# Optimization experiments

Hardware: AMD Instinct MI355X
Metric: run time of the kernel (lower is better)

## Reference

```python
import jax, jax.numpy as jnp
import numpy as np

B, F, N_SP, VIS_DIM, DIM, HEADS = 2, 16, 784, 512, 512, 8


def setup_inputs() -> dict:
    key = jax.random.key(0)
    k0, k1, k2 = jax.random.split(key, 3)
    x = jax.random.normal(k0, (B, F * N_SP, VIS_DIM), dtype=jnp.float32)
    # QKV: nn.Linear(vis_dim, dim*3, bias=False) -> weight [3*dim, vis_dim]
    Wqkv = jax.random.normal(k1, (3 * DIM, VIS_DIM), dtype=jnp.float32) * 0.02
    # proj: nn.Linear(dim, vis_dim) -> weight [vis_dim, dim], bias [vis_dim]
    Wproj = jax.random.normal(k2, (VIS_DIM, DIM), dtype=jnp.float32) * 0.02
    bproj = jnp.zeros((VIS_DIM,), dtype=jnp.float32)
    return {"x": x, "Wqkv": Wqkv, "Wproj": Wproj, "bproj": bproj,
            "spatial": N_SP, "f": F, "n": N_SP}


def reference(x, Wqkv, Wproj, bproj, spatial, f, n):
    # Factorized (divided space-time) SPATIAL attention:
    # einops_from='b (f n) d', einops_to='(b f) n d' -- attention over n within each frame.
    h = HEADS
    b, seq, _ = x.shape  # seq = f * n
    dim = Wqkv.shape[0] // 3
    hd = dim // h
    scale = hd ** -0.5

    qkv = x @ Wqkv.T                             # [b, f*n, 3*dim]
    q, k, v = jnp.split(qkv, 3, axis=-1)
    rs = lambda t: t.reshape(b, f, n, h, hd)     # b (f n) (h d) -> b f n h d
    q = rs(q) * scale
    k = rs(k)
    v = rs(v)

    # scores over spatial tokens within each (batch, frame, head)
    attn = jax.nn.softmax(jnp.einsum('bfihd,bfjhd->bfhij', q, k), axis=-1)
    out = jnp.einsum('bfhij,bfjhd->bfihd', attn, v)   # [b, f, n, h, hd]
    out = out.reshape(b, seq, dim)               # merge heads + restore (f n)
    return out @ Wproj.T + bproj                 # [b, f*n, vis_dim]
```

## Files before the change

### kernel.cpp

```cpp
#include <hip/hip_runtime.h>
#include <hip/hip_bf16.h>
#include <stdint.h>

using bf16 = __hip_bfloat16;
typedef __bf16 bf16x8 __attribute__((ext_vector_type(8)));
typedef float f32x4  __attribute__((ext_vector_type(4)));
typedef float f32x16 __attribute__((ext_vector_type(16)));

#define NB 2
#define NF 16
#define NSP 784
#define SEQ 12544
#define MROWS 25088
#define QSCALE 0.18033688011112042f

__device__ inline void gload16(const void* g, void* l) {
    __builtin_amdgcn_global_load_lds(
        (const __attribute__((address_space(1))) unsigned int*)g,
        (__attribute__((address_space(3))) unsigned int*)l, 16, 0, 0);
}
__device__ inline ushort f2bu(float x) {
    union { bf16 b; ushort u; } c; c.b = __float2bfloat16(x); return c.u;
}

__global__ __launch_bounds__(256)
void cvt_x_kernel(const float* __restrict__ x, ushort* __restrict__ xb, int n4) {
    int i = blockIdx.x * 256 + threadIdx.x;
    int stride = gridDim.x * 256;
    for (; i < n4; i += stride) {
        float4 v = ((const float4*)x)[i];
        ushort4 u;
        u.x = f2bu(v.x); u.y = f2bu(v.y); u.z = f2bu(v.z); u.w = f2bu(v.w);
        ((ushort4*)xb)[i] = u;
    }
}

__global__ __launch_bounds__(256)
void cvt_w_kernel(const float* __restrict__ wqkv, const float* __restrict__ wproj,
                  ushort* __restrict__ wqkvb, ushort* __restrict__ wpb) {
    int i = blockIdx.x * 256 + threadIdx.x;
    float4 v;
    ushort4 u;
    if (i < 196608) {
        float s = (i < 65536) ? QSCALE : 1.0f;
        v = ((const float4*)wqkv)[i];
        u.x = f2bu(v.x * s); u.y = f2bu(v.y * s);
        u.z = f2bu(v.z * s); u.w = f2bu(v.w * s);
        ((ushort4*)wqkvb)[i] = u;
    } else {
        int j = i - 196608;
        v = ((const float4*)wproj)[j];
        u.x = f2bu(v.x); u.y = f2bu(v.y); u.z = f2bu(v.z); u.w = f2bu(v.w);
        ((ushort4*)wpb)[j] = u;
    }
}

template<int EPI>
__global__ __launch_bounds__(256)
void gemm_mfma(const ushort* __restrict__ A, const ushort* __restrict__ W,
               const float* __restrict__ bias, ushort* __restrict__ outb,
               float* __restrict__ outf, int K, int ldc, int npan)
{
    constexpr int BK  = 64;
    constexpr int SWZ = 7;
    __shared__ ushort smem[16384];

    const int tid = threadIdx.x;
    const int bid = blockIdx.x;
    const int gsz = 4 * npan;
    const int r   = bid % gsz;
    const int m0 = ((bid / gsz) * 4 + (r & 3)) * 128;
    const int n0 = (r >> 2) * 128;
    const int l  = tid & 63;
    const int wv = tid >> 6;
    const int wm = wv >> 1, wn = wv & 1;
    const int lm = l & 15;
    const int koffb = (l >> 4) * 16;
    const int swz = (lm & SWZ) << 4;

    const int rsub = tid >> 3;
    const int cb0  = (tid & 7) * 16;
    const int wofs = (tid >> 6) * 512;

    const size_t ldb = (size_t)K * 2;
    const char* Ab = (const char*)A + (size_t)m0 * ldb;
    const char* Wb = (const char*)W + (size_t)n0 * ldb;

    f32x4 acc[4][4] = {};

    for (int k0 = 0; k0 < K; k0 += BK) {
        if (k0) __syncthreads();
#pragma unroll
        for (int i = 0; i < 4; ++i) {
            int row = i * 32 + rsub;
            int cbs = cb0 ^ ((row & SWZ) << 4);
            size_t roff = (size_t)row * ldb + (size_t)(k0 * 2 + cbs);
            gload16(Ab + roff, smem +        i * 2048 + wofs);
            gload16(Wb + roff, smem + 8192 + i * 2048 + wofs);
        }
        __syncthreads();

#pragma unroll
        for (int ks = 0; ks < 2; ++ks) {
            bf16x8 af[4], wf[4];
            const int cb = ((ks * 64 + koffb) ^ swz) >> 1;
#pragma unroll
            for (int f = 0; f < 4; ++f) {
                int rA = wm * 64 + f * 16 + lm;
                int rW = wn * 64 + f * 16 + lm;
                af[f] = *(const bf16x8*)&smem[rA * BK + cb];
                wf[f] = *(const bf16x8*)&smem[8192 + rW * BK + cb];
            }
            __builtin_amdgcn_s_setprio(1);
#pragma unroll
            for (int fm = 0; fm < 4; ++fm)
#pragma unroll
                for (int fn = 0; fn < 4; ++fn)
                    acc[fm][fn] = __builtin_amdgcn_mfma_f32_16x16x32_bf16(
                        wf[fn], af[fm], acc[fm][fn], 0, 0, 0);
            __builtin_amdgcn_s_setprio(0);
        }
    }

    const int ln4 = (l >> 4) * 4;
    if (EPI == 0) {
#pragma unroll
        for (int fm = 0; fm < 4; ++fm) {
            int m = m0 + wm * 64 + fm * 16 + lm;
            ushort* rowp = outb + (size_t)m * ldc + n0 + wn * 64 + ln4;
#pragma unroll
            for (int fn = 0; fn < 4; ++fn) {
                ushort4 u;
                u.x = f2bu(acc[fm][fn][0]); u.y = f2bu(acc[fm][fn][1]);
                u.z = f2bu(acc[fm][fn][2]); u.w = f2bu(acc[fm][fn][3]);
                *(ushort4*)(rowp + fn * 16) = u;
            }
        }
    } else {
#pragma unroll
        for (int fm = 0; fm < 4; ++fm) {
            int m = m0 + wm * 64 + fm * 16 + lm;
            float* rowp = outf + (size_t)m * ldc + n0 + wn * 64 + ln4;
#pragma unroll
            for (int fn = 0; fn < 4; ++fn) {
                float4 b4 = *(const float4*)&bias[n0 + wn * 64 + fn * 16 + ln4];
                float4 o;
                o.x = acc[fm][fn][0] + b4.x; o.y = acc[fm][fn][1] + b4.y;
                o.z = acc[fm][fn][2] + b4.z; o.w = acc[fm][fn][3] + b4.w;
                *(float4*)(rowp + fn * 16) = o;
            }
        }
    }
}

__global__ __launch_bounds__(256)
void vtrans(const ushort* __restrict__ qkv, ushort* __restrict__ vt)
{
    __shared__ __align__(16) ushort T[256][72];
    const int tid = threadIdx.x;
    const int pr  = blockIdx.x;
    const int c   = blockIdx.y;
    const int hh  = pr & 7, bfi = pr >> 3;
    const ushort* vsrc = qkv + (size_t)bfi * NSP * 1536 + 1024 + hh * 64;
    ushort* dst = vt + (size_t)pr * (64 * NSP);
    const int d = tid & 63, q = tid >> 6;

    const int j0 = c * 256;
    const int nj = (NSP - j0) < 256 ? (NSP - j0) : 256;
    if (tid < nj) {
        const ushort* src = vsrc + (size_t)(j0 + tid) * 1536;
#pragma unroll
        for (int u = 0; u < 8; ++u)
            *(uint4*)&T[tid][u * 8] = *(const uint4*)(src + u * 8);
    }
    __syncthreads();
    if (q * 64 < nj) {
        int cnt = nj - q * 64; if (cnt > 64) cnt = 64;
        union { uint4 u[8]; ushort s[64]; } buf;
#pragma unroll
        for (int jj = 0; jj < 64; ++jj)
            buf.s[jj] = T[q * 64 + jj][d];
        ushort* o = dst + (size_t)d * NSP + j0 + q * 64;
        if (cnt == 64) {
#pragma unroll
            for (int u = 0; u < 8; ++u) *(uint4*)(o + u * 8) = buf.u[u];
        } else {
#pragma unroll
            for (int u = 0; u < 2; ++u) *(uint4*)(o + u * 8) = buf.u[u];
        }
    }
}

__global__ __launch_bounds__(256, 4)
void attn_mfma(const ushort* __restrict__ qkv, const ushort* __restrict__ vt,
               ushort* __restrict__ oh)
{
    __shared__ __align__(16) ushort Ks[2][4096];
    __shared__ __align__(16) ushort Vs[2][4096];
    const int tid = threadIdx.x;
    const int l   = tid & 63;
    const int li  = l & 31;
    const int h5  = l >> 5;
    const int w   = tid >> 6;

    const int bid  = blockIdx.x;
    const int xcd  = bid & 7;
    const int slot = bid >> 3;
    const int pr   = (xcd << 5) + slot / 7;
    const int qt   = slot % 7;
    const int hh   = pr & 7;
    const int bfi  = pr >> 3;
    const size_t rowbase = (size_t)bfi * NSP;
    const int iq = qt * 128 + w * 32 + li;
    const bool qvalid = iq < NSP;
    const int iqc = qvalid ? iq : NSP - 1;

    bf16x8 qf[4];
    {
        const ushort* qrow = qkv + (rowbase + iqc) * 1536 + hh * 64 + h5 * 8;
#pragma unroll
        for (int ks = 0; ks < 4; ++ks)
            qf[ks] = *(const bf16x8*)(qrow + ks * 16);
    }

    const char* kb0   = (const char*)(qkv + rowbase * 1536 + 512 + hh * 64);
    const char* vbase = (const char*)(vt + (size_t)pr * (64 * NSP));

    const int srow = tid >> 3;
    const int sg16 = (tid & 7) * 16;
    const int sswz = sg16 ^ ((srow & 7) << 4);

    f32x16 o0 = {}, o1 = {}, dacc = {};
    const f32x16 fz = {};
    bf16x8 onesf;
    {
        union { ushort u[8]; bf16x8 v; } one_;
#pragma unroll
        for (int e = 0; e < 8; ++e) one_.u[e] = 0x3F80;
        onesf = one_.v;
    }

    const int rsw   = (li & 7) << 4;
    const int base0 = li * 128;
    const int base1 = (32 + li) * 128;

#pragma unroll
    for (int i = 0; i < 2; ++i) {
        int row = i * 32 + srow;
        gload16(kb0 + (size_t)row * 3072 + sswz, &Ks[0][i * 2048 + tid * 8]);
        gload16(vbase + (size_t)row * 1568 + sswz, &Vs[0][i * 2048 + tid * 8]);
    }
    __syncthreads();

    const char* kp0 = kb0 + (size_t)(64 + srow) * 3072 + sswz;
    const char* kp1 = kb0 + (size_t)(96 + srow) * 3072 + sswz;
    const char* vp0 = vbase + (size_t)srow * 1568 + 128 + sswz;
    const char* vp1 = vbase + (size_t)(32 + srow) * 1568 + 128 + sswz;

    int cur = 0;
    for (int t = 0; t < 13; ++t) {
        if (t < 11) {
            gload16(kp0, &Ks[cur ^ 1][tid * 8]);
            gload16(kp1, &Ks[cur ^ 1][2048 + tid * 8]);
            gload16(vp0, &Vs[cur ^ 1][tid * 8]);
            gload16(vp1, &Vs[cur ^ 1][2048 + tid * 8]);
            kp0 += 196608; kp1 += 196608;
            vp0 += 128;    vp1 += 128;
        } else if (t == 11) {
#pragma unroll
            for (int i = 0; i < 2; ++i) {
                int row = i * 32 + srow;
                int jr = 768 + row; if (jr > NSP - 1) jr = NSP - 1;
                gload16(kb0 + (size_t)jr * 3072 + sswz, &Ks[cur ^ 1][i * 2048 + tid * 8]);
                int cb = 1536 + sswz;
                if (cb + 16 > NSP * 2) cb = 1536;
                gload16(vbase + (size_t)row * 1568 + cb, &Vs[cur ^ 1][i * 2048 + tid * 8]);
            }
        }

        const char* KsC = (const char*)&Ks[cur][0];
        const char* VsC = (const char*)&Vs[cur][0];

        f32x16 s0, s1;
        __builtin_amdgcn_s_setprio(1);
        {
            int cb = (h5 * 16) ^ rsw;
            bf16x8 k0 = *(const bf16x8*)(KsC + base0 + cb);
            bf16x8 k1 = *(const bf16x8*)(KsC + base1 + cb);
            s0 = __builtin_amdgcn_mfma_f32_32x32x16_bf16(k0, qf[0], fz, 0, 0, 0);
            s1 = __builtin_amdgcn_mfma_f32_32x32x16_bf16(k1, qf[0], fz, 0, 0, 0);
        }
#pragma unroll
        for (int ks = 1; ks < 4; ++ks) {
            int cb = (ks * 32 + h5 * 16) ^ rsw;
            bf16x8 k0 = *(const bf16x8*)(KsC + base0 + cb);
            bf16x8 k1 = *(const bf16x8*)(KsC + base1 + cb);
            s0 = __builtin_amdgcn_mfma_f32_32x32x16_bf16(k0, qf[ks], s0, 0, 0, 0);
            s1 = __builtin_amdgcn_mfma_f32_32x32x16_bf16(k1, qf[ks], s1, 0, 0, 0);
        }
        __builtin_amdgcn_s_setprio(0);

        if (t == 12) {
#pragma unroll
            for (int r = 0; r < 16; ++r) {
                int jl = (r & 3) + 8 * (r >> 2) + 4 * h5;
                if (768 + jl >= NSP)      s0[r] = -1e30f;
                if (768 + 32 + jl >= NSP) s1[r] = -1e30f;
            }
        }

#pragma unroll
        for (int r = 0; r < 16; ++r) { s0[r] = exp2f(s0[r]); s1[r] = exp2f(s1[r]); }

#pragma unroll
        for (int js = 0; js < 4; ++js) {
            const int rb8 = (js & 1) * 8;
            const f32x16& s = (js < 2) ? s0 : s1;
            uint A0, A1, B0, B1;
            asm("v_cvt_pk_bf16_f32 %0, %1, %2" : "=v"(A0) : "v"(s[rb8+0]), "v"(s[rb8+1]));
            asm("v_cvt_pk_bf16_f32 %0, %1, %2" : "=v"(A1) : "v"(s[rb8+2]), "v"(s[rb8+3]));
            asm("v_cvt_pk_bf16_f32 %0, %1, %2" : "=v"(B0) : "v"(s[rb8+4]), "v"(s[rb8+5]));
            asm("v_cvt_pk_bf16_f32 %0, %1, %2" : "=v"(B1) : "v"(s[rb8+6]), "v"(s[rb8+7]));
            asm volatile("v_permlane32_swap_b32 %0, %1" : "+v"(A0), "+v"(B0));
            asm volatile("v_permlane32_swap_b32 %0, %1" : "+v"(A1), "+v"(B1));
            union { uint u[4]; bf16x8 v; } pf;
            pf.u[0] = A0; pf.u[1] = A1; pf.u[2] = B0; pf.u[3] = B1;

            int cb = (js * 32 + h5 * 16) ^ rsw;
            bf16x8 v0f = *(const bf16x8*)(VsC + base0 + cb);
            bf16x8 v1f = *(const bf16x8*)(VsC + base1 + cb);
            __builtin_amdgcn_s_setprio(1);
            o0   = __builtin_amdgcn_mfma_f32_32x32x16_bf16(v0f, pf.v, o0, 0, 0, 0);
            o1   = __builtin_amdgcn_mfma_f32_32x32x16_bf16(v1f, pf.v, o1, 0, 0, 0);
            dacc = __builtin_amdgcn_mfma_f32_32x32x16_bf16(onesf, pf.v, dacc, 0, 0, 0);
            __builtin_amdgcn_s_setprio(0);
        }

        __syncthreads();
        cur ^= 1;
    }

    if (qvalid) {
        float inv = 1.0f / dacc[0];
        size_t ro = (rowbase + iq) * 512 + hh * 64;
#pragma unroll
        for (int g = 0; g < 4; ++g) {
            int d = g * 8 + h5 * 4;
            ushort4 uh0, uh1;
#pragma unroll
            for (int m = 0; m < 4; ++m) {
                ((ushort*)&uh0)[m] = f2bu(o0[g * 4 + m] * inv);
                ((ushort*)&uh1)[m] = f2bu(o1[g * 4 + m] * inv);
            }
            *(ushort4*)&oh[ro + d]      = uh0;
            *(ushort4*)&oh[ro + 32 + d] = uh1;
        }
    }
}

extern "C" void kernel_launch(void* const* d_in, const int* in_sizes, int n_in,
                              void* d_out, int out_size, void* d_ws, size_t ws_size,
                              hipStream_t stream) {
    const float* x     = (const float*)d_in[0];
    const float* Wqkv  = (const float*)d_in[1];
    const float* Wproj = (const float*)d_in[2];
    const float* bproj = (const float*)d_in[3];
    float* out = (float*)d_out;

    char* ws = (char*)d_ws;
    ushort* xb_ah = (ushort*)(ws);
    ushort* qkvb  = (ushort*)(ws + 25690112);
    ushort* wqkvb = (ushort*)(ws + 102760448);
    ushort* wpb   = (ushort*)(ws + 104333312);

    ushort* vtb = (ushort*)d_out;

    dim3 blk(256);
    cvt_x_kernel<<<2048, blk, 0, stream>>>(x, xb_ah, (MROWS * 512) / 4);
    cvt_w_kernel<<<1024, blk, 0, stream>>>(Wqkv, Wproj, wqkvb, wpb);

    gemm_mfma<0><<<dim3(2352), blk, 0, stream>>>(
        xb_ah, wqkvb, nullptr, qkvb, nullptr, 512, 1536, 12);

    vtrans<<<dim3(256, 4), blk, 0, stream>>>(qkvb, vtb);

    attn_mfma<<<dim3(1792), blk, 0, stream>>>(qkvb, vtb, xb_ah);

    gemm_mfma<1><<<dim3(784), blk, 0, stream>>>(
        xb_ah, wpb, bproj, nullptr, out, 512, 512, 4);
}
```

Measured before the change: 220.7 us.

## Triple-buffer K/V tiles in attention kernel with partial vmcnt waits

Replaces the double-buffered K/V LDS pipeline with a three-stage ring, prefetching two tiles ahead. Barriers now wait with s_waitcnt vmcnt(4) rather than a full __syncthreads drain, so one tile's loads can stay in flight across the barrier. This is meant to hide global load latency better. In exchange, LDS use grows by half and occupancy drops from 4 to 3 blocks per CU. There is also some ordering risk because the final iteration skips its barrier.

New measurement: 219.8 us. Within noise of the previous version (-0.4%).

```diff
diff --git a/kernel.cpp b/kernel.cpp
--- a/kernel.cpp
+++ b/kernel.cpp
@@ -191,12 +191,12 @@
     }
 }
 
-__global__ __launch_bounds__(256, 4)
+__global__ __launch_bounds__(256, 3)
 void attn_mfma(const ushort* __restrict__ qkv, const ushort* __restrict__ vt,
                ushort* __restrict__ oh)
 {
-    __shared__ __align__(16) ushort Ks[2][4096];
-    __shared__ __align__(16) ushort Vs[2][4096];
+    __shared__ __align__(16) ushort Ks[3][4096];
+    __shared__ __align__(16) ushort Vs[3][4096];
     const int tid = threadIdx.x;
     const int l   = tid & 63;
     const int li  = l & 31;
@@ -245,41 +245,47 @@
     const int base1 = (32 + li) * 128;
 
 #pragma unroll
-    for (int i = 0; i < 2; ++i) {
-        int row = i * 32 + srow;
-        gload16(kb0 + (size_t)row * 3072 + sswz, &Ks[0][i * 2048 + tid * 8]);
-        gload16(vbase + (size_t)row * 1568 + sswz, &Vs[0][i * 2048 + tid * 8]);
-    }
-    __syncthreads();
-
-    const char* kp0 = kb0 + (size_t)(64 + srow) * 3072 + sswz;
-    const char* kp1 = kb0 + (size_t)(96 + srow) * 3072 + sswz;
-    const char* vp0 = vbase + (size_t)srow * 1568 + 128 + sswz;
-    const char* vp1 = vbase + (size_t)(32 + srow) * 1568 + 128 + sswz;
-
-    int cur = 0;
+    for (int u = 0; u < 2; ++u) {
+#pragma unroll
+        for (int i = 0; i < 2; ++i) {
+            int row = u * 64 + i * 32 + srow;
+            gload16(kb0 + (size_t)row * 3072 + sswz, &Ks[u][i * 2048 + tid * 8]);
+            gload16(vbase + (size_t)(i * 32 + srow) * 1568 + u * 128 + sswz,
+                    &Vs[u][i * 2048 + tid * 8]);
+        }
+    }
+    asm volatile("s_waitcnt vmcnt(4)" ::: "memory");
+    __builtin_amdgcn_s_barrier();
+
+    const char* kp0 = kb0 + (size_t)(128 + srow) * 3072 + sswz;
+    const char* kp1 = kb0 + (size_t)(160 + srow) * 3072 + sswz;
+    const char* vp0 = vbase + (size_t)srow * 1568 + 256 + sswz;
+    const char* vp1 = vbase + (size_t)(32 + srow) * 1568 + 256 + sswz;
+
+    int rd = 0;
     for (int t = 0; t < 13; ++t) {
-        if (t < 11) {
-            gload16(kp0, &Ks[cur ^ 1][tid * 8]);
-            gload16(kp1, &Ks[cur ^ 1][2048 + tid * 8]);
-            gload16(vp0, &Vs[cur ^ 1][tid * 8]);
-            gload16(vp1, &Vs[cur ^ 1][2048 + tid * 8]);
+        int st = rd + 2; if (st >= 3) st -= 3;
+        if (t <= 9) {
+            gload16(kp0, &Ks[st][tid * 8]);
+            gload16(kp1, &Ks[st][2048 + tid * 8]);
+            gload16(vp0, &Vs[st][tid * 8]);
+            gload16(vp1, &Vs[st][2048 + tid * 8]);
             kp0 += 196608; kp1 += 196608;
             vp0 += 128;    vp1 += 128;
-        } else if (t == 11) {
+        } else if (t == 10) {
 #pragma unroll
             for (int i = 0; i < 2; ++i) {
                 int row = i * 32 + srow;
                 int jr = 768 + row; if (jr > NSP - 1) jr = NSP - 1;
-                gload16(kb0 + (size_t)jr * 3072 + sswz, &Ks[cur ^ 1][i * 2048 + tid * 8]);
+                gload16(kb0 + (size_t)jr * 3072 + sswz, &Ks[st][i * 2048 + tid * 8]);
                 int cb = 1536 + sswz;
                 if (cb + 16 > NSP * 2) cb = 1536;
-                gload16(vbase + (size_t)row * 1568 + cb, &Vs[cur ^ 1][i * 2048 + tid * 8]);
-            }
-        }
-
-        const char* KsC = (const char*)&Ks[cur][0];
-        const char* VsC = (const char*)&Vs[cur][0];
+                gload16(vbase + (size_t)row * 1568 + cb, &Vs[st][i * 2048 + tid * 8]);
+            }
+        }
+
+        const char* KsC = (const char*)&Ks[rd][0];
+        const char* VsC = (const char*)&Vs[rd][0];
 
         f32x16 s0, s1;
         __builtin_amdgcn_s_setprio(1);
@@ -336,8 +342,12 @@
             __builtin_amdgcn_s_setprio(0);
         }
 
-        __syncthreads();
-        cur ^= 1;
+        if (t < 12) {
+            if (t <= 10) asm volatile("s_waitcnt vmcnt(4)" ::: "memory");
+            else         asm volatile("s_waitcnt vmcnt(0)" ::: "memory");
+            __builtin_amdgcn_s_barrier();
+        }
+        rd = rd + 1; if (rd >= 3) rd = 0;
     }
 
     if (qvalid) {
```
